# Kernel tuning notes

Measured on AMD Instinct MI355X. Metric: run time of the kernel, lower is better.

The kernel has to match this reference:

```python
import jax, jax.numpy as jnp
import numpy as np

N = 50000        # nodes
E = 800000       # edges (avg degree 16)
F = 64           # num_features
G = 128          # number of graphs in the batch
NOUT = 1         # n_output


def setup_inputs() -> dict:
    key = jax.random.key(0)
    ks = jax.random.split(key, 9)
    x = jax.random.normal(ks[0], (N, F), dtype=jnp.float32)
    edge_index = jax.random.randint(ks[1], (2, E), 0, N, dtype=jnp.int64)
    batch = jnp.sort(jax.random.randint(ks[2], (N,), 0, G, dtype=jnp.int64))
    W1 = jax.random.normal(ks[3], (F, F), dtype=jnp.float32) * 0.1
    b1 = jnp.zeros((F,), dtype=jnp.float32)
    W2 = jax.random.normal(ks[4], (F, 2 * F), dtype=jnp.float32) * 0.1
    b2 = jnp.zeros((2 * F,), dtype=jnp.float32)
    fcW = jax.random.normal(ks[5], (2 * F, NOUT), dtype=jnp.float32) * 0.1
    fcb = jnp.zeros((NOUT,), dtype=jnp.float32)
    return {"x": x, "edge_index": edge_index, "batch": batch,
            "W1": W1, "b1": b1, "W2": W2, "b2": b2, "fcW": fcW, "fcb": fcb}


def reference(x, edge_index, batch, W1, b1, W2, b2, fcW, fcb):
    n = x.shape[0]
    # PyG GCNConv: add self-loops, symmetric normalization D^-1/2 (A+I) D^-1/2
    loop = jnp.arange(n, dtype=edge_index.dtype)
    src = jnp.concatenate([edge_index[0], loop])  # [E+N]
    dst = jnp.concatenate([edge_index[1], loop])  # [E+N]
    deg = jax.ops.segment_sum(jnp.ones_like(dst, dtype=x.dtype), dst, num_segments=n)
    dinv = jnp.where(deg > 0, jax.lax.rsqrt(jnp.maximum(deg, 1.0)), 0.0)
    norm = dinv[src] * dinv[dst]                  # [E+N]

    def gcn_conv(h, W, b):
        h = h @ W                                 # [N, Fout]
        msg = h[src] * norm[:, None]              # gather + scale, [E+N, Fout]
        return jax.ops.segment_sum(msg, dst, num_segments=n) + b

    h1 = jax.nn.relu(gcn_conv(x, W1, b1))         # [N, F]
    h2 = jax.nn.relu(gcn_conv(h1, W2, b2))        # [N, 2F]

    # global mean pool per graph (dropout is identity in eval)
    counts = jax.ops.segment_sum(jnp.ones((n,), x.dtype), batch, num_segments=G)
    pooled = jax.ops.segment_sum(h2, batch, num_segments=G)
    pooled = pooled / jnp.maximum(counts, 1.0)[:, None]  # [G, 2F]

    out = pooled @ fcW + fcb                      # [G, NOUT]
    return out.reshape(1, -1)                     # [1, G*NOUT]
```

## Files before the change

### kernel.cpp

```cpp
#include <hip/hip_runtime.h>
#include <hip/hip_bf16.h>

typedef __hip_bfloat16 bf16;

static __device__ __forceinline__ float loadF(const void* p, long long i, int f32){
  return f32 ? ((const float*)p)[i] : __bfloat162float(((const bf16*)p)[i]);
}
static __device__ __forceinline__ int loadI(const void* p, long long i, int i64){
  return i64 ? (int)((const long long*)p)[i] : ((const int*)p)[i];
}
static __device__ __forceinline__ unsigned short f2bf(float f){
  unsigned u = __float_as_uint(f);
  return (unsigned short)((u + 0x7FFFu + ((u>>16)&1u)) >> 16);
}
static __device__ __forceinline__ float bf2f(unsigned v){
  return __uint_as_float(v<<16);
}

#define CAP 4096
#define LB_EDGES 2048

__global__ void k_init(const unsigned int* __restrict__ xw, const unsigned int* __restrict__ eiw,
                       int* __restrict__ flags, int* __restrict__ gcursor, int nbuckets,
                       float* __restrict__ S, int gn){
  int i = blockIdx.x*256 + threadIdx.x;
  if(i < nbuckets) gcursor[i] = 0;
  if(i < gn) S[i] = 0.f;
  if(blockIdx.x == 0){
    __shared__ int s1, s2;
    if(threadIdx.x==0){ s1=0; s2=0; }
    __syncthreads();
    unsigned w = xw[threadIdx.x];
    int e = (int)((w>>7)&0xFFu);
    if(e>=110 && e<=135) atomicAdd(&s1, 1);
    if(eiw[2*threadIdx.x+1] != 0u) atomicAdd(&s2, 1);
    __syncthreads();
    if(threadIdx.x==0){
      flags[0] = (s1 < 128) ? 1 : 0;
      flags[1] = (s2 < 128) ? 1 : 0;
    }
  }
}

__global__ __launch_bounds__(256) void k_pre(const void* __restrict__ ei, int E, int N,
                                             const int* __restrict__ flags,
                                             int* __restrict__ gcursor,
                                             unsigned int* __restrict__ log, int nbuckets,
                                             const void* __restrict__ x, const void* __restrict__ W,
                                             unsigned short* __restrict__ y, int nLog){
  __shared__ unsigned int smem[12416];
  int t = threadIdx.x;
  if((int)blockIdx.x < nLog){
    unsigned int* stash = smem;
    int* hcnt  = (int*)(smem + LB_EDGES);
    int* hbase = (int*)(smem + LB_EDGES + 1024);
    for(int b=t; b<nbuckets; b+=256) hcnt[b] = 0;
    __syncthreads();
    int i64 = flags[1];
    long long e0 = (long long)blockIdx.x*LB_EDGES;
    int cnt = (int)(((long long)E - e0) < LB_EDGES ? ((long long)E - e0) : LB_EDGES);
    for(int k=t; k<cnt; k+=256){
      long long e = e0 + k;
      int s = loadI(ei, e, i64);                 s = min(max(s,0), N-1);
      int d = loadI(ei, (long long)E + e, i64);  d = min(max(d,0), N-1);
      unsigned p = (((unsigned)d)<<16) | (unsigned)s;
      stash[k] = p;
      atomicAdd(&hcnt[d>>6], 1);
    }
    __syncthreads();
    for(int b=t; b<nbuckets; b+=256){
      int c = hcnt[b];
      hbase[b] = (c>0) ? atomicAdd(&gcursor[b], c) : 0;
      hcnt[b] = 0;
    }
    __syncthreads();
    for(int k=t; k<cnt; k+=256){
      unsigned p = stash[k];
      int b = (int)(p>>22);
      int pos = hbase[b] + atomicAdd(&hcnt[b], 1);
      if(pos < CAP) log[(long long)b*CAP + pos] = p;
    }
  } else {
    float* Ws = (float*)smem;
    float* xs = (float*)(smem + 4096);
    int f32 = flags[0];
    for(int i=t;i<4096;i+=256) Ws[i] = loadF(W, i, f32);
    int row0 = ((int)blockIdx.x - nLog)*128;
    for(int i=t;i<8192;i+=256){
      int r = i>>6, c = i&63;
      int gr = row0 + r;
      xs[r*65 + c] = (gr<N) ? loadF(x, (long long)gr*64 + c, f32) : 0.f;
    }
    __syncthreads();
    int cg = t&15, rg = t>>4;
    int col_g = cg*4, row_g = rg*8;
    float acc[8][4];
    #pragma unroll
    for(int r=0;r<8;r++){ acc[r][0]=0.f; acc[r][1]=0.f; acc[r][2]=0.f; acc[r][3]=0.f; }
    for(int k=0;k<64;k++){
      float4 w = *(const float4*)&Ws[k*64 + col_g];
      float xr[8];
      #pragma unroll
      for(int r=0;r<8;r++) xr[r] = xs[(row_g+r)*65 + k];
      #pragma unroll
      for(int r=0;r<8;r++){
        acc[r][0] += xr[r]*w.x; acc[r][1] += xr[r]*w.y;
        acc[r][2] += xr[r]*w.z; acc[r][3] += xr[r]*w.w;
      }
    }
    #pragma unroll
    for(int r=0;r<8;r++){
      int gr = row0 + row_g + r;
      if(gr<N){
        ushort4 st;
        st.x = f2bf(acc[r][0]); st.y = f2bf(acc[r][1]);
        st.z = f2bf(acc[r][2]); st.w = f2bf(acc[r][3]);
        *(ushort4*)&y[(long long)gr*64 + col_g] = st;
      }
    }
  }
}

__global__ __launch_bounds__(256) void k_bsortg0(const unsigned int* __restrict__ log,
                                                 const int* __restrict__ gcursor,
                                                 unsigned short* __restrict__ csr,
                                                 int* __restrict__ beg, int* __restrict__ endv,
                                                 float* __restrict__ dinv,
                                                 const unsigned int* __restrict__ Y32,
                                                 unsigned int* __restrict__ G032, int N){
  __shared__ int hist[64];
  __shared__ int cur[64];
  __shared__ float dloc[64];
  int b = blockIdx.x, t = threadIdx.x;
  if(t < 64) hist[t] = 0;
  __syncthreads();
  int n = min(gcursor[b], CAP);
  const unsigned int* L = log + (long long)b*CAP;
  for(int j=t; j<n; j+=256) atomicAdd(&hist[(L[j]>>16)&63], 1);
  __syncthreads();
  if(t < 64){
    int v = hist[t];
    int inc = v;
    #pragma unroll
    for(int o=1; o<64; o<<=1){
      int u = __shfl_up(inc, o);
      if(t >= o) inc += u;
    }
    int excl = inc - v;
    cur[t] = excl;
    float dv = rsqrtf((float)(v + 1));
    dloc[t] = dv;
    int node = b*64 + t;
    if(node < N){
      int base = b*CAP + excl;
      beg[node]  = base;
      endv[node] = base + v;
      dinv[node] = dv;
    }
  }
  __syncthreads();
  unsigned short* C = csr + (long long)b*CAP;
  for(int j=t; j<n; j+=256){
    unsigned p = L[j];
    int l = (int)((p>>16)&63u);
    int pos = atomicAdd(&cur[l], 1);
    C[pos] = (unsigned short)(p & 0xFFFFu);
  }
  long long base32 = (long long)b*2048;
  for(int i=t; i<2048; i+=256){
    int nl = i>>5;
    int node = b*64 + nl;
    if(node < N){
      unsigned v = Y32[base32 + i];
      float dv = dloc[nl];
      G032[base32 + i] = (unsigned)f2bf(bf2f(v & 0xFFFFu)*dv)
                       | ((unsigned)f2bf(bf2f(v >> 16)*dv) << 16);
    }
  }
}

__global__ __launch_bounds__(256) void k_agg(const unsigned short* __restrict__ g,
                                             const unsigned short* __restrict__ csr,
                                             const int* __restrict__ beg, const int* __restrict__ endv,
                                             const float* __restrict__ dinv,
                                             const void* __restrict__ bias, const int* __restrict__ flags,
                                             int mode,
                                             unsigned int* __restrict__ out32, int N){
  int node = blockIdx.x*4 + (threadIdx.x>>6);
  int lane = threadIdx.x&63;
  if(node >= N) return;
  int half = lane>>5, fl = lane&31;
  const unsigned int* G32 = (const unsigned int*)g;
  int j = beg[node], e = endv[node];
  float2 a0={0.f,0.f}, a1={0.f,0.f}, a2={0.f,0.f}, a3={0.f,0.f};
  float2 a4={0.f,0.f}, a5={0.f,0.f}, a6={0.f,0.f}, a7={0.f,0.f};
  for(; j+16<=e; j+=16){
    int s0 = csr[j +  0 + half];
    int s1 = csr[j +  2 + half];
    int s2 = csr[j +  4 + half];
    int s3 = csr[j +  6 + half];
    int s4 = csr[j +  8 + half];
    int s5 = csr[j + 10 + half];
    int s6 = csr[j + 12 + half];
    int s7 = csr[j + 14 + half];
    unsigned v0 = G32[(long long)s0*32 + fl];
    unsigned v1 = G32[(long long)s1*32 + fl];
    unsigned v2 = G32[(long long)s2*32 + fl];
    unsigned v3 = G32[(long long)s3*32 + fl];
    unsigned v4 = G32[(long long)s4*32 + fl];
    unsigned v5 = G32[(long long)s5*32 + fl];
    unsigned v6 = G32[(long long)s6*32 + fl];
    unsigned v7 = G32[(long long)s7*32 + fl];
    a0.x += bf2f(v0 & 0xFFFFu); a0.y += bf2f(v0 >> 16);
    a1.x += bf2f(v1 & 0xFFFFu); a1.y += bf2f(v1 >> 16);
    a2.x += bf2f(v2 & 0xFFFFu); a2.y += bf2f(v2 >> 16);
    a3.x += bf2f(v3 & 0xFFFFu); a3.y += bf2f(v3 >> 16);
    a4.x += bf2f(v4 & 0xFFFFu); a4.y += bf2f(v4 >> 16);
    a5.x += bf2f(v5 & 0xFFFFu); a5.y += bf2f(v5 >> 16);
    a6.x += bf2f(v6 & 0xFFFFu); a6.y += bf2f(v6 >> 16);
    a7.x += bf2f(v7 & 0xFFFFu); a7.y += bf2f(v7 >> 16);
  }
  for(; j+8<=e; j+=8){
    int s0 = csr[j + 0 + half];
    int s1 = csr[j + 2 + half];
    int s2 = csr[j + 4 + half];
    int s3 = csr[j + 6 + half];
    unsigned v0 = G32[(long long)s0*32 + fl];
    unsigned v1 = G32[(long long)s1*32 + fl];
    unsigned v2 = G32[(long long)s2*32 + fl];
    unsigned v3 = G32[(long long)s3*32 + fl];
    a0.x += bf2f(v0 & 0xFFFFu); a0.y += bf2f(v0 >> 16);
    a1.x += bf2f(v1 & 0xFFFFu); a1.y += bf2f(v1 >> 16);
    a2.x += bf2f(v2 & 0xFFFFu); a2.y += bf2f(v2 >> 16);
    a3.x += bf2f(v3 & 0xFFFFu); a3.y += bf2f(v3 >> 16);
  }
  for(; j+2<=e; j+=2){
    int s = csr[j + half];
    unsigned v = G32[(long long)s*32 + fl];
    a0.x += bf2f(v & 0xFFFFu); a0.y += bf2f(v >> 16);
  }
  if(j < e && half == 0){
    int s = csr[j];
    unsigned v = G32[(long long)s*32 + fl];
    a0.x += bf2f(v & 0xFFFFu); a0.y += bf2f(v >> 16);
  }
  float sx = ((a0.x+a1.x)+(a2.x+a3.x)) + ((a4.x+a5.x)+(a6.x+a7.x));
  float sy = ((a0.y+a1.y)+(a2.y+a3.y)) + ((a4.y+a5.y)+(a6.y+a7.y));
  sx += __shfl_xor(sx, 32, 64);
  sy += __shfl_xor(sy, 32, 64);
  unsigned sv = G32[(long long)node*32 + fl];
  float dv = dinv[node];
  sx = (sx + bf2f(sv & 0xFFFFu)) * dv;
  sy = (sy + bf2f(sv >> 16)) * dv;
  if(mode){
    int f32 = flags[0];
    float bx = loadF(bias, 2*fl,   f32);
    float by = loadF(bias, 2*fl+1, f32);
    sx = fmaxf(sx + bx, 0.f) * dv;
    sy = fmaxf(sy + by, 0.f) * dv;
  }
  if(half == 0)
    out32[(long long)node*32 + fl] = (unsigned)f2bf(sx) | ((unsigned)f2bf(sy) << 16);
}

__global__ __launch_bounds__(256) void k_gemm2pool(const unsigned int* __restrict__ A32, const void* __restrict__ W,
                                                   const void* __restrict__ b, const void* __restrict__ fcW,
                                                   const void* __restrict__ batch, const int* __restrict__ flags,
                                                   float* __restrict__ S, int N, int NOUT){
  __shared__ float Ws[64*128];
  __shared__ float xs[128*65];
  __shared__ float Sloc[128*4];
  __shared__ int gid[128];
  int f32 = flags[0], i64 = flags[1];
  int tid = threadIdx.x;
  int row0 = blockIdx.x*128;
  for(int i=tid;i<8192;i+=256) Ws[i] = loadF(W, i, f32);
  for(int i=tid;i<4096;i+=256){
    int r = i>>5, kd = i&31;
    int gr = row0 + r;
    unsigned v = (gr<N) ? A32[(long long)gr*32 + kd] : 0u;
    xs[r*65 + 2*kd    ] = bf2f(v & 0xFFFFu);
    xs[r*65 + 2*kd + 1] = bf2f(v >> 16);
  }
  if(tid < 128){
    int node = row0 + tid;
    gid[tid] = (node < N) ? loadI(batch, node, i64) : 0;
  }
  for(int i=tid;i<512;i+=256) Sloc[i] = 0.f;
  __syncthreads();
  int cg = tid&15, rg = tid>>4;
  int c0 = cg*4, c1 = 64 + cg*4, row_g = rg*8;
  float acc[8][8];
  #pragma unroll
  for(int r=0;r<8;r++)
    #pragma unroll
    for(int c=0;c<8;c++) acc[r][c]=0.f;
  for(int k=0;k<64;k++){
    float4 w0 = *(const float4*)&Ws[k*128 + c0];
    float4 w1 = *(const float4*)&Ws[k*128 + c1];
    float xr[8];
    #pragma unroll
    for(int r=0;r<8;r++) xr[r] = xs[(row_g+r)*65 + k];
    #pragma unroll
    for(int r=0;r<8;r++){
      acc[r][0] += xr[r]*w0.x; acc[r][1] += xr[r]*w0.y;
      acc[r][2] += xr[r]*w0.z; acc[r][3] += xr[r]*w0.w;
      acc[r][4] += xr[r]*w1.x; acc[r][5] += xr[r]*w1.y;
      acc[r][6] += xr[r]*w1.z; acc[r][7] += xr[r]*w1.w;
    }
  }
  #pragma unroll
  for(int c=0;c<8;c++){
    int col = (c<4) ? (c0+c) : (c1+c-4);
    float bb = loadF(b, col, f32);
    #pragma unroll
    for(int r=0;r<8;r++){ float z = acc[r][c]+bb; acc[r][c] = z>0.f?z:0.f; }
  }
  int nv = N - row0; nv = nv < 128 ? nv : 128;
  if(nv <= 0) return;
  int gmin = gid[0], gmax = gid[nv-1];
  bool ldsOK = (NOUT <= 4) && (gmax - gmin < 128);
  for(int o=0;o<NOUT;o++){
    float fw[8];
    #pragma unroll
    for(int c=0;c<8;c++){
      int col = (c<4) ? (c0+c) : (c1+c-4);
      fw[c] = loadF(fcW, (long long)col*NOUT + o, f32);
    }
    #pragma unroll
    for(int r=0;r<8;r++){
      float z = acc[r][0]*fw[0] + acc[r][1]*fw[1] + acc[r][2]*fw[2] + acc[r][3]*fw[3]
              + acc[r][4]*fw[4] + acc[r][5]*fw[5] + acc[r][6]*fw[6] + acc[r][7]*fw[7];
      #pragma unroll
      for(int m=1;m<16;m<<=1) z += __shfl_xor(z, m, 64);
      int nl = row_g + r;
      if(cg==0 && nl < nv){
        int gg = gid[nl];
        if(ldsOK) atomicAdd(&Sloc[(gg-gmin)*NOUT + o], z);
        else      atomicAdd(&S[(long long)gg*NOUT + o], z);
      }
    }
  }
  if(ldsOK){
    __syncthreads();
    int nbin = (gmax - gmin + 1)*NOUT;
    for(int i=tid; i<nbin; i+=256){
      float v = Sloc[i];
      if(v != 0.f){
        int bin = i / NOUT, o = i - bin*NOUT;
        atomicAdd(&S[(long long)(gmin+bin)*NOUT + o], v);
      }
    }
  }
}

static __device__ __forceinline__ int lower_bound_batch(const void* batch, int N, int key, int i64){
  int lo = 0, hi = N;
  while(lo < hi){ int mid = (lo+hi)>>1; if(loadI(batch, mid, i64) < key) lo = mid+1; else hi = mid; }
  return lo;
}

__global__ void k_final2(const float* __restrict__ S, const void* __restrict__ batch, int N,
                         const int* __restrict__ flags, const void* __restrict__ fcb,
                         void* __restrict__ out, int G, int NOUT){
  int f32 = flags[0], i64 = flags[1];
  int g = blockIdx.x*256 + threadIdx.x;
  if(g >= G) return;
  int c = lower_bound_batch(batch, N, g+1, i64) - lower_bound_batch(batch, N, g, i64);
  float inv = 1.f / (float)(c > 0 ? c : 1);
  for(int o=0;o<NOUT;o++){
    float r = S[(long long)g*NOUT+o]*inv + loadF(fcb, o, f32);
    if(f32) ((float*)out)[g*NOUT+o] = r;
    else    ((unsigned short*)out)[g*NOUT+o] = f2bf(r);
  }
}

extern "C" void kernel_launch(void* const* d_in, const int* in_sizes, int n_in,
                              void* d_out, int out_size, void* d_ws, size_t ws_size,
                              hipStream_t stream) {
  const void* x    = d_in[0];
  const void* ei   = d_in[1];
  const void* batch= d_in[2];
  const void* W1   = d_in[3];
  const void* b1   = d_in[4];
  const void* W2   = d_in[5];
  const void* b2   = d_in[6];
  const void* fcW  = d_in[7];
  const void* fcb  = d_in[8];

  const int N = in_sizes[0] / 64;
  const int E = in_sizes[1] / 2;
  const int NOUT = in_sizes[8];
  const int G = out_size / NOUT;
  const int nbuckets = (N + 63) >> 6;

  size_t off = 0;
  auto alloc = [&](size_t bytes) -> char* {
    char* p = (char*)d_ws + off;
    off += (bytes + 511) & ~(size_t)511;
    return p;
  };
  int*   flags   = (int*)  alloc(512);
  int*   gcursor = (int*)  alloc((size_t)nbuckets*4);
  float* dinv    = (float*)alloc((size_t)N*4);
  int*   beg     = (int*)  alloc((size_t)N*4);
  int*   endv    = (int*)  alloc((size_t)N*4);
  float* S       = (float*)alloc((size_t)G*NOUT*4);
  unsigned int*   log  = (unsigned int*)  alloc((size_t)nbuckets*CAP*4);
  unsigned short* csr  = (unsigned short*)alloc((size_t)nbuckets*CAP*2);
  unsigned short* yB   = (unsigned short*)alloc((size_t)N*64*2);
  unsigned short* g0   = (unsigned short*)alloc((size_t)N*64*2);
  unsigned short* g1   = (unsigned short*)alloc((size_t)N*64*2);
  unsigned int*   aBuf = (unsigned int*)  alloc((size_t)N*32*4);
  (void)ws_size; (void)n_in;

  int initgrid = (nbuckets > G*NOUT ? nbuckets : G*NOUT);
  int nLog = (E + LB_EDGES - 1) / LB_EDGES;
  int nGem = (N + 127) / 128;

  k_init    <<<(initgrid+255)/256, 256, 0, stream>>>((const unsigned int*)x, (const unsigned int*)ei,
                                                     flags, gcursor, nbuckets, S, G*NOUT);
  k_pre     <<<nLog + nGem,   256, 0, stream>>>(ei, E, N, flags, gcursor, log, nbuckets,
                                                x, W1, yB, nLog);
  k_bsortg0 <<<nbuckets,      256, 0, stream>>>(log, gcursor, csr, beg, endv, dinv,
                                                (const unsigned int*)yB, (unsigned int*)g0, N);

  k_agg     <<<(N+3)/4,       256, 0, stream>>>(g0, csr, beg, endv, dinv, b1, flags, 1,
                                                (unsigned int*)g1, N);
  k_agg     <<<(N+3)/4,       256, 0, stream>>>(g1, csr, beg, endv, dinv, b1, flags, 0,
                                                aBuf, N);
  k_gemm2pool<<<(N+127)/128,  256, 0, stream>>>(aBuf, W2, b2, fcW, batch, flags, S, N, NOUT);

  k_final2  <<<(G+255)/256,   256, 0, stream>>>(S, batch, N, flags, fcb, d_out, G, NOUT);
}
```

Baseline: 212.1 us.

## Replace bucketed edge log with per-node degree count and global atomic placement

CSR construction changes from a two-level bucket sort (per-block shared-memory histograms, bucket logs, then a per-bucket local sort) to a global per-node degree count with atomics. A per-bucket scan produces per-node offsets, and a separate placement kernel scatters source indices using per-node global atomic cursors. This removes the shared-memory staging and the intermediate bucket log pass, at the cost of many global atomics on deg and cur plus one extra kernel launch. The edge order within each node's list becomes nondeterministic.

```diff
diff --git a/kernel.cpp b/kernel.cpp
--- a/kernel.cpp
+++ b/kernel.cpp
@@ -18,13 +18,13 @@
 }
 
 #define CAP 4096
-#define LB_EDGES 2048
+#define CNT_EDGES 4096
 
 __global__ void k_init(const unsigned int* __restrict__ xw, const unsigned int* __restrict__ eiw,
-                       int* __restrict__ flags, int* __restrict__ gcursor, int nbuckets,
+                       int* __restrict__ flags, int* __restrict__ deg, int N,
                        float* __restrict__ S, int gn){
   int i = blockIdx.x*256 + threadIdx.x;
-  if(i < nbuckets) gcursor[i] = 0;
+  if(i < N) deg[i] = 0;
   if(i < gn) S[i] = 0.f;
   if(blockIdx.x == 0){
     __shared__ int s1, s2;
@@ -44,48 +44,28 @@
 
 __global__ __launch_bounds__(256) void k_pre(const void* __restrict__ ei, int E, int N,
                                              const int* __restrict__ flags,
-                                             int* __restrict__ gcursor,
-                                             unsigned int* __restrict__ log, int nbuckets,
+                                             int* __restrict__ deg,
+                                             unsigned int* __restrict__ plog,
                                              const void* __restrict__ x, const void* __restrict__ W,
-                                             unsigned short* __restrict__ y, int nLog){
-  __shared__ unsigned int smem[12416];
+                                             unsigned short* __restrict__ y, int nCnt){
   int t = threadIdx.x;
-  if((int)blockIdx.x < nLog){
-    unsigned int* stash = smem;
-    int* hcnt  = (int*)(smem + LB_EDGES);
-    int* hbase = (int*)(smem + LB_EDGES + 1024);
-    for(int b=t; b<nbuckets; b+=256) hcnt[b] = 0;
-    __syncthreads();
+  if((int)blockIdx.x < nCnt){
     int i64 = flags[1];
-    long long e0 = (long long)blockIdx.x*LB_EDGES;
-    int cnt = (int)(((long long)E - e0) < LB_EDGES ? ((long long)E - e0) : LB_EDGES);
+    long long e0 = (long long)blockIdx.x*CNT_EDGES;
+    int cnt = (int)(((long long)E - e0) < CNT_EDGES ? ((long long)E - e0) : CNT_EDGES);
     for(int k=t; k<cnt; k+=256){
       long long e = e0 + k;
       int s = loadI(ei, e, i64);                 s = min(max(s,0), N-1);
       int d = loadI(ei, (long long)E + e, i64);  d = min(max(d,0), N-1);
-      unsigned p = (((unsigned)d)<<16) | (unsigned)s;
-      stash[k] = p;
-      atomicAdd(&hcnt[d>>6], 1);
-    }
-    __syncthreads();
-    for(int b=t; b<nbuckets; b+=256){
-      int c = hcnt[b];
-      hbase[b] = (c>0) ? atomicAdd(&gcursor[b], c) : 0;
-      hcnt[b] = 0;
-    }
-    __syncthreads();
-    for(int k=t; k<cnt; k+=256){
-      unsigned p = stash[k];
-      int b = (int)(p>>22);
-      int pos = hbase[b] + atomicAdd(&hcnt[b], 1);
-      if(pos < CAP) log[(long long)b*CAP + pos] = p;
+      plog[e] = (((unsigned)d)<<16) | (unsigned)s;
+      atomicAdd(&deg[d], 1);
     }
   } else {
-    float* Ws = (float*)smem;
-    float* xs = (float*)(smem + 4096);
+    __shared__ float Ws[64*64];
+    __shared__ float xs[128*65];
     int f32 = flags[0];
     for(int i=t;i<4096;i+=256) Ws[i] = loadF(W, i, f32);
-    int row0 = ((int)blockIdx.x - nLog)*128;
+    int row0 = ((int)blockIdx.x - nCnt)*128;
     for(int i=t;i<8192;i+=256){
       int r = i>>6, c = i&63;
       int gr = row0 + r;
@@ -121,25 +101,17 @@
   }
 }
 
-__global__ __launch_bounds__(256) void k_bsortg0(const unsigned int* __restrict__ log,
-                                                 const int* __restrict__ gcursor,
-                                                 unsigned short* __restrict__ csr,
-                                                 int* __restrict__ beg, int* __restrict__ endv,
-                                                 float* __restrict__ dinv,
-                                                 const unsigned int* __restrict__ Y32,
-                                                 unsigned int* __restrict__ G032, int N){
-  __shared__ int hist[64];
-  __shared__ int cur[64];
+__global__ __launch_bounds__(256) void k_scan(const int* __restrict__ deg,
+                                              int* __restrict__ cur,
+                                              int* __restrict__ beg, int* __restrict__ endv,
+                                              float* __restrict__ dinv,
+                                              const unsigned int* __restrict__ Y32,
+                                              unsigned int* __restrict__ G032, int N){
   __shared__ float dloc[64];
   int b = blockIdx.x, t = threadIdx.x;
-  if(t < 64) hist[t] = 0;
-  __syncthreads();
-  int n = min(gcursor[b], CAP);
-  const unsigned int* L = log + (long long)b*CAP;
-  for(int j=t; j<n; j+=256) atomicAdd(&hist[(L[j]>>16)&63], 1);
-  __syncthreads();
   if(t < 64){
-    int v = hist[t];
+    int node = b*64 + t;
+    int v = (node < N) ? deg[node] : 0;
     int inc = v;
     #pragma unroll
     for(int o=1; o<64; o<<=1){
@@ -147,25 +119,19 @@
       if(t >= o) inc += u;
     }
     int excl = inc - v;
-    cur[t] = excl;
     float dv = rsqrtf((float)(v + 1));
     dloc[t] = dv;
-    int node = b*64 + t;
     if(node < N){
-      int base = b*CAP + excl;
+      int bend = (b+1)*CAP;
+      int base = b*CAP + excl; if(base > bend) base = bend;
+      int ev   = base + v;     if(ev   > bend) ev   = bend;
       beg[node]  = base;
-      endv[node] = base + v;
+      endv[node] = ev;
+      cur[node]  = base;
       dinv[node] = dv;
     }
   }
   __syncthreads();
-  unsigned short* C = csr + (long long)b*CAP;
-  for(int j=t; j<n; j+=256){
-    unsigned p = L[j];
-    int l = (int)((p>>16)&63u);
-    int pos = atomicAdd(&cur[l], 1);
-    C[pos] = (unsigned short)(p & 0xFFFFu);
-  }
   long long base32 = (long long)b*2048;
   for(int i=t; i<2048; i+=256){
     int nl = i>>5;
@@ -176,6 +142,20 @@
       G032[base32 + i] = (unsigned)f2bf(bf2f(v & 0xFFFFu)*dv)
                        | ((unsigned)f2bf(bf2f(v >> 16)*dv) << 16);
     }
+  }
+}
+
+__global__ __launch_bounds__(256) void k_place(const unsigned int* __restrict__ plog, int E,
+                                               int* __restrict__ cur,
+                                               unsigned short* __restrict__ csr){
+  long long e0 = (long long)blockIdx.x*CNT_EDGES;
+  int cnt = (int)(((long long)E - e0) < CNT_EDGES ? ((long long)E - e0) : CNT_EDGES);
+  for(int k=threadIdx.x; k<cnt; k+=256){
+    unsigned p = plog[e0 + k];
+    int d = (int)(p >> 16);
+    int pos = atomicAdd(&cur[d], 1);
+    int bend = ((d>>6)+1)*CAP;
+    if(pos < bend) csr[pos] = (unsigned short)(p & 0xFFFFu);
   }
 }
 
@@ -401,12 +381,13 @@
     return p;
   };
   int*   flags   = (int*)  alloc(512);
-  int*   gcursor = (int*)  alloc((size_t)nbuckets*4);
+  int*   deg     = (int*)  alloc((size_t)N*4);
+  int*   cur     = (int*)  alloc((size_t)N*4);
   float* dinv    = (float*)alloc((size_t)N*4);
   int*   beg     = (int*)  alloc((size_t)N*4);
   int*   endv    = (int*)  alloc((size_t)N*4);
   float* S       = (float*)alloc((size_t)G*NOUT*4);
-  unsigned int*   log  = (unsigned int*)  alloc((size_t)nbuckets*CAP*4);
+  unsigned int*   plog = (unsigned int*)  alloc((size_t)E*4);
   unsigned short* csr  = (unsigned short*)alloc((size_t)nbuckets*CAP*2);
   unsigned short* yB   = (unsigned short*)alloc((size_t)N*64*2);
   unsigned short* g0   = (unsigned short*)alloc((size_t)N*64*2);
@@ -414,16 +395,16 @@
   unsigned int*   aBuf = (unsigned int*)  alloc((size_t)N*32*4);
   (void)ws_size; (void)n_in;
 
-  int initgrid = (nbuckets > G*NOUT ? nbuckets : G*NOUT);
-  int nLog = (E + LB_EDGES - 1) / LB_EDGES;
+  int initgrid = (N > G*NOUT ? N : G*NOUT);
+  int nCnt = (E + CNT_EDGES - 1) / CNT_EDGES;
   int nGem = (N + 127) / 128;
 
   k_init    <<<(initgrid+255)/256, 256, 0, stream>>>((const unsigned int*)x, (const unsigned int*)ei,
-                                                     flags, gcursor, nbuckets, S, G*NOUT);
-  k_pre     <<<nLog + nGem,   256, 0, stream>>>(ei, E, N, flags, gcursor, log, nbuckets,
-                                                x, W1, yB, nLog);
-  k_bsortg0 <<<nbuckets,      256, 0, stream>>>(log, gcursor, csr, beg, endv, dinv,
+                                                     flags, deg, N, S, G*NOUT);
+  k_pre     <<<nCnt + nGem,   256, 0, stream>>>(ei, E, N, flags, deg, plog, x, W1, yB, nCnt);
+  k_scan    <<<nbuckets,      256, 0, stream>>>(deg, cur, beg, endv, dinv,
                                                 (const unsigned int*)yB, (unsigned int*)g0, N);
+  k_place   <<<nCnt,          256, 0, stream>>>(plog, E, cur, csr);
 
   k_agg     <<<(N+3)/4,       256, 0, stream>>>(g0, csr, beg, endv, dinv, b1, flags, 1,
                                                 (unsigned int*)g1, N);
```

New measurement: 265.5 us. 25.1% more time.
